# Kernel tuning notes

Measured on AMD Instinct MI355X. Metric: run time of the kernel, lower is better.

Reference implementation:

```python
import jax, jax.numpy as jnp
import numpy as np

N = 50000      # nodes
E = 800000     # edges
XS = 64        # x_size
ES = 32        # edge_attr dim (in_size = XS + ES = 96)
OUT = 64       # out_size
H = 128        # hidden_size
EPS = 1e-5


def _lin_init(k, fan_in, fan_out):
    s = 1.0 / np.sqrt(fan_in)
    kw, kb = jax.random.split(k)
    w = jax.random.uniform(kw, (fan_in, fan_out), minval=-s, maxval=s, dtype=jnp.float32)
    b = jax.random.uniform(kb, (fan_out,), minval=-s, maxval=s, dtype=jnp.float32)
    return w, b


def setup_inputs() -> dict:
    key = jax.random.key(0)
    ks = jax.random.split(key, 12)
    x = jax.random.normal(ks[0], (N, XS), dtype=jnp.float32)
    edge_index = jax.random.randint(ks[1], (2, E), 0, N, dtype=jnp.int64)
    edge_attr = jax.random.normal(ks[2], (E, ES), dtype=jnp.float32)
    u = jax.random.normal(ks[3], (1, 8), dtype=jnp.float32)
    batch = jnp.zeros((N,), dtype=jnp.int64)
    # MLP1: (96->128) LReLU (128->128) LReLU (128->64) LReLU LN(64)
    m1w0, m1b0 = _lin_init(ks[4], XS + ES, H)
    m1w1, m1b1 = _lin_init(ks[5], H, H)
    m1w2, m1b2 = _lin_init(ks[6], H, OUT)
    ln1_g = jnp.ones((OUT,), jnp.float32); ln1_b = jnp.zeros((OUT,), jnp.float32)
    # MLP2: (128->128) LReLU (128->128) LReLU (128->64) LReLU LN(64)
    m2w0, m2b0 = _lin_init(ks[7], XS + OUT, H)
    m2w1, m2b1 = _lin_init(ks[8], H, H)
    m2w2, m2b2 = _lin_init(ks[9], H, OUT)
    ln2_g = jnp.ones((OUT,), jnp.float32); ln2_b = jnp.zeros((OUT,), jnp.float32)
    return dict(x=x, edge_index=edge_index, edge_attr=edge_attr, u=u, batch=batch,
                m1w0=m1w0, m1b0=m1b0, m1w1=m1w1, m1b1=m1b1, m1w2=m1w2, m1b2=m1b2,
                ln1_g=ln1_g, ln1_b=ln1_b,
                m2w0=m2w0, m2b0=m2b0, m2w1=m2w1, m2b1=m2b1, m2w2=m2w2, m2b2=m2b2,
                ln2_g=ln2_g, ln2_b=ln2_b)


def _lrelu(v):
    return jax.nn.leaky_relu(v, 0.01)


def _layernorm(v, g, b):
    mu = jnp.mean(v, axis=-1, keepdims=True)
    var = jnp.mean(jnp.square(v - mu), axis=-1, keepdims=True)
    return (v - mu) * jax.lax.rsqrt(var + EPS) * g + b


def _mlp(h, w0, b0, w1, b1, w2, b2, g, bn):
    h = _lrelu(h @ w0 + b0)
    h = _lrelu(h @ w1 + b1)
    h = _lrelu(h @ w2 + b2)          # activate_last=True
    return _layernorm(h, g, bn)      # layer_norm=True


def reference(x, edge_index, edge_attr, u, batch,
              m1w0, m1b0, m1w1, m1b1, m1w2, m1b2, ln1_g, ln1_b,
              m2w0, m2b0, m2w1, m2b1, m2w2, m2b2, ln2_g, ln2_b):
    row, col = edge_index[0], edge_index[1]
    # gather source nodes, concat edge features -> per-edge MLP
    h = jnp.concatenate([x[row], edge_attr], axis=1)            # [E, 96]
    h = _mlp(h, m1w0, m1b0, m1w1, m1b1, m1w2, m1b2, ln1_g, ln1_b)  # [E, 64]
    # scatter_mean over destination nodes
    agg = jax.ops.segment_sum(h, col, num_segments=N)           # [N, 64]
    cnt = jax.ops.segment_sum(jnp.ones((E,), h.dtype), col, num_segments=N)
    agg = agg / jnp.maximum(cnt, 1.0)[:, None]
    # node update MLP
    h2 = jnp.concatenate([x, agg], axis=1)                      # [N, 128]
    return _mlp(h2, m2w0, m2b0, m2w1, m2b1, m2w2, m2b2, ln2_g, ln2_b)
```

## Files before the change

### kernel.cpp

```cpp
#include <hip/hip_runtime.h>


#define NNODES 50000
#define NEDGES 800000
#define NTILES_E 6250
#define NTILES_N 391

typedef __bf16 bf16;
typedef __bf16 __attribute__((ext_vector_type(4))) bf16x4;
typedef __bf16 __attribute__((ext_vector_type(8))) bf16x8;
typedef float __attribute__((ext_vector_type(4))) f32x4;

__device__ __forceinline__ f32x4 mfma_bf16(bf16x8 a, bf16x8 b, f32x4 c) {
    return __builtin_amdgcn_mfma_f32_16x16x32_bf16(a, b, c, 0, 0, 0);
}

__global__ void prep_weights(const float* __restrict__ w10, const float* __restrict__ w11,
                             const float* __restrict__ w12, const float* __restrict__ w20,
                             const float* __restrict__ w21, const float* __restrict__ w22,
                             bf16* __restrict__ img) {
    int idx = blockIdx.x * 256 + threadIdx.x;
    float f;
    if (idx < 13312) {
        int n = idx / 104, k = idx % 104;
        f = (k < 96) ? w10[k * 128 + n] : 0.0f;
    } else if (idx < 30720) {
        int t = idx - 13312; int n = t / 136, k = t % 136;
        f = (k < 128) ? w11[k * 128 + n] : 0.0f;
    } else if (idx < 39424) {
        int t = idx - 30720; int n = t / 136, k = t % 136;
        f = (k < 128) ? w12[k * 64 + n] : 0.0f;
    } else if (idx < 56832) {
        int t = idx - 39424; int n = t / 136, k = t % 136;
        f = (k < 128) ? w20[k * 128 + n] : 0.0f;
    } else if (idx < 74240) {
        int t = idx - 56832; int n = t / 136, k = t % 136;
        f = (k < 128) ? w21[k * 128 + n] : 0.0f;
    } else if (idx < 82944) {
        int t = idx - 74240; int n = t / 136, k = t % 136;
        f = (k < 128) ? w22[k * 64 + n] : 0.0f;
    } else {
        return;
    }
    img[idx] = (bf16)f;
}

__global__ void hist_kernel(const int* __restrict__ col, int* __restrict__ hist) {
    int i = blockIdx.x * 512 + threadIdx.x;
    if (i < NEDGES) atomicAdd(hist + col[i], 1);
}

__global__ void scanA(const int* __restrict__ hist, int* __restrict__ off,
                      int* __restrict__ csum) {
    __shared__ int sd[512];
    int t = threadIdx.x, i = blockIdx.x * 512 + t;
    int v = (i < NNODES) ? hist[i] : 0;
    sd[t] = v;
    __syncthreads();
    for (int o2 = 1; o2 < 512; o2 <<= 1) {
        int x = (t >= o2) ? sd[t - o2] : 0;
        __syncthreads();
        sd[t] += x;
        __syncthreads();
    }
    if (i < NNODES) off[i] = sd[t] - v;
    if (t == 511) csum[blockIdx.x] = sd[511];
}

__global__ void scanB(int* __restrict__ csum) {
    __shared__ int sd[128];
    int t = threadIdx.x;
    int v = (t < 98) ? csum[t] : 0;
    sd[t] = v;
    __syncthreads();
    for (int o2 = 1; o2 < 128; o2 <<= 1) {
        int x = (t >= o2) ? sd[t - o2] : 0;
        __syncthreads();
        sd[t] += x;
        __syncthreads();
    }
    if (t < 98) csum[t] = sd[t] - v;
}

__global__ void scanC(int* __restrict__ off, const int* __restrict__ csum) {
    int i = blockIdx.x * 512 + threadIdx.x;
    if (i < NNODES) off[i] += csum[blockIdx.x];
}

__global__ void scatter_kernel(const int* __restrict__ eidx, int* __restrict__ off,
                               int* __restrict__ perm, int* __restrict__ rdS) {
    int i = blockIdx.x * 512 + threadIdx.x;
    if (i < NEDGES) {
        int r = eidx[i], d = eidx[NEDGES + i];
        int pos = atomicAdd(off + d, 1);
        perm[pos] = i;
        rdS[pos] = r | (d << 16);
    }
}

__global__ __launch_bounds__(256) void edge_mlp(
    const float* __restrict__ x, const int* __restrict__ perm,
    const int* __restrict__ rdS, const float* __restrict__ eattr,
    const bf16* __restrict__ wimg,
    const float* __restrict__ b0g, const float* __restrict__ b1g,
    const float* __restrict__ b2g, const float* __restrict__ lng,
    const float* __restrict__ lnb, float* __restrict__ agg) {
    __shared__ __align__(16) bf16 wall[39424];
    __shared__ __align__(16) bf16 atile[128 * 104];
    __shared__ __align__(16) bf16 hid[128 * 136];
    __shared__ float bs[448];
    __shared__ int dstile[128];

    const int tid = threadIdx.x;
    {
        const uint4* src = (const uint4*)wimg;
        uint4* dst = (uint4*)wall;
        for (int i = tid; i < 4928; i += 256) dst[i] = src[i];
    }
    if (tid < 128) { bs[tid] = b0g[tid]; bs[128 + tid] = b1g[tid]; }
    else {
        int t = tid - 128;
        if (t < 64) { bs[256 + t] = b2g[t]; bs[320 + t] = lng[t]; bs[384 + t] = lnb[t]; }
    }
    __syncthreads();

    const int lane = tid & 63;
    const int wv = tid >> 6;
    const int col16 = lane & 15;
    const int quad = lane >> 4;

    float b0r[8], b1r[8], b2r[4], gr[4], br[4];
#pragma unroll
    for (int i = 0; i < 8; i++) { b0r[i] = bs[i * 16 + col16]; b1r[i] = bs[128 + i * 16 + col16]; }
#pragma unroll
    for (int i = 0; i < 4; i++) {
        b2r[i] = bs[256 + i * 16 + col16];
        gr[i] = bs[320 + i * 16 + col16];
        br[i] = bs[384 + i * 16 + col16];
    }

    const bf16* w0t = wall;
    const bf16* w1t = wall + 13312;
    const bf16* w2t = wall + 30720;

    const f32x4 vzero = {0.0f, 0.0f, 0.0f, 0.0f};
    const int r0 = wv * 32 + col16;
    const int rw = wv * 32 + quad * 4;
    const int el = tid >> 1, half = tid & 1;

    for (int tile = blockIdx.x; tile < NTILES_E; tile += gridDim.x) {
        const int sbase = tile * 128;
        {
            const int s = sbase + el;
            const int v = rdS[s];
            const int e = perm[s];
            const int r = v & 0xFFFF;
            if (half == 0) dstile[el] = ((unsigned)v) >> 16;
            const float4* xs = (const float4*)(x + (size_t)r * 64);
            bf16* arow = atile + el * 104;
#pragma unroll
            for (int j = 0; j < 8; j++) {
                float4 vv = xs[half * 8 + j];
                bf16x4 u = {(bf16)vv.x, (bf16)vv.y, (bf16)vv.z, (bf16)vv.w};
                *(bf16x4*)(arow + half * 32 + j * 4) = u;
            }
            const float4* es = (const float4*)(eattr + (size_t)e * 32);
#pragma unroll
            for (int j = 0; j < 4; j++) {
                float4 vv = es[half * 4 + j];
                bf16x4 u = {(bf16)vv.x, (bf16)vv.y, (bf16)vv.z, (bf16)vv.w};
                *(bf16x4*)(arow + 64 + half * 16 + j * 4) = u;
            }
        }

        f32x4 acc1[2][8];
#pragma unroll
        for (int mt = 0; mt < 2; mt++)
#pragma unroll
            for (int nt = 0; nt < 8; nt++) acc1[mt][nt] = vzero;
#pragma unroll
        for (int ks = 0; ks < 3; ks++) {
            bf16x8 a0 = *(const bf16x8*)(atile + r0 * 104 + ks * 32 + quad * 8);
            bf16x8 a1 = *(const bf16x8*)(atile + (r0 + 16) * 104 + ks * 32 + quad * 8);
#pragma unroll
            for (int nt = 0; nt < 8; nt++) {
                bf16x8 b = *(const bf16x8*)(w0t + (nt * 16 + col16) * 104 + ks * 32 + quad * 8);
                acc1[0][nt] = mfma_bf16(a0, b, acc1[0][nt]);
                acc1[1][nt] = mfma_bf16(a1, b, acc1[1][nt]);
            }
        }
#pragma unroll
        for (int mt = 0; mt < 2; mt++)
#pragma unroll
            for (int nt = 0; nt < 8; nt++)
#pragma unroll
                for (int rg = 0; rg < 4; rg++) {
                    float v = acc1[mt][nt][rg] + b0r[nt];
                    v = (v > 0.0f) ? v : 0.01f * v;
                    hid[(rw + mt * 16 + rg) * 136 + nt * 16 + col16] = (bf16)v;
                }

        bf16x8 a2[2][4];
#pragma unroll
        for (int mt = 0; mt < 2; mt++)
#pragma unroll
            for (int ks = 0; ks < 4; ks++)
                a2[mt][ks] = *(const bf16x8*)(hid + (r0 + mt * 16) * 136 + ks * 32 + quad * 8);
        f32x4 acc2[2][8];
#pragma unroll
        for (int mt = 0; mt < 2; mt++)
#pragma unroll
            for (int nt = 0; nt < 8; nt++) acc2[mt][nt] = vzero;
#pragma unroll
        for (int ks = 0; ks < 4; ks++) {
#pragma unroll
            for (int nt = 0; nt < 8; nt++) {
                bf16x8 b = *(const bf16x8*)(w1t + (nt * 16 + col16) * 136 + ks * 32 + quad * 8);
                acc2[0][nt] = mfma_bf16(a2[0][ks], b, acc2[0][nt]);
                acc2[1][nt] = mfma_bf16(a2[1][ks], b, acc2[1][nt]);
            }
        }
#pragma unroll
        for (int mt = 0; mt < 2; mt++)
#pragma unroll
            for (int nt = 0; nt < 8; nt++)
#pragma unroll
                for (int rg = 0; rg < 4; rg++) {
                    float v = acc2[mt][nt][rg] + b1r[nt];
                    v = (v > 0.0f) ? v : 0.01f * v;
                    hid[(rw + mt * 16 + rg) * 136 + nt * 16 + col16] = (bf16)v;
                }

        bf16x8 a3[2][4];
#pragma unroll
        for (int mt = 0; mt < 2; mt++)
#pragma unroll
            for (int ks = 0; ks < 4; ks++)
                a3[mt][ks] = *(const bf16x8*)(hid + (r0 + mt * 16) * 136 + ks * 32 + quad * 8);
        f32x4 acc3[2][4];
#pragma unroll
        for (int mt = 0; mt < 2; mt++)
#pragma unroll
            for (int nt = 0; nt < 4; nt++) acc3[mt][nt] = vzero;
#pragma unroll
        for (int ks = 0; ks < 4; ks++) {
#pragma unroll
            for (int nt = 0; nt < 4; nt++) {
                bf16x8 b = *(const bf16x8*)(w2t + (nt * 16 + col16) * 136 + ks * 32 + quad * 8);
                acc3[0][nt] = mfma_bf16(a3[0][ks], b, acc3[0][nt]);
                acc3[1][nt] = mfma_bf16(a3[1][ks], b, acc3[1][nt]);
            }
        }

#pragma unroll
        for (int mt = 0; mt < 2; mt++) {
            float vals[4][4];
            float s1[4] = {0.f, 0.f, 0.f, 0.f}, s2[4] = {0.f, 0.f, 0.f, 0.f};
#pragma unroll
            for (int nt = 0; nt < 4; nt++)
#pragma unroll
                for (int rg = 0; rg < 4; rg++) {
                    float v = acc3[mt][nt][rg] + b2r[nt];
                    v = (v > 0.0f) ? v : 0.01f * v;
                    vals[nt][rg] = v;
                    s1[rg] += v;
                    s2[rg] += v * v;
                }
#pragma unroll
            for (int off2 = 1; off2 < 16; off2 <<= 1) {
#pragma unroll
                for (int rg = 0; rg < 4; rg++) {
                    s1[rg] += __shfl_xor(s1[rg], off2);
                    s2[rg] += __shfl_xor(s2[rg], off2);
                }
            }
            float o[4][4];
            int dr[4];
#pragma unroll
            for (int rg = 0; rg < 4; rg++) {
                float mu = s1[rg] * 0.015625f;
                float var = s2[rg] * 0.015625f - mu * mu;
                float rstd = rsqrtf(var + 1e-5f);
                dr[rg] = dstile[rw + mt * 16 + rg];
#pragma unroll
                for (int nt = 0; nt < 4; nt++)
                    o[nt][rg] = (vals[nt][rg] - mu) * rstd * gr[nt] + br[nt];
            }
            float run0 = o[0][0], run1 = o[1][0], run2 = o[2][0], run3 = o[3][0];
            int cur = dr[0];
#pragma unroll
            for (int rg = 1; rg < 4; rg++) {
                if (dr[rg] != cur) {
                    float* dst = agg + (size_t)cur * 64 + col16;
                    atomicAdd(dst, run0); atomicAdd(dst + 16, run1);
                    atomicAdd(dst + 32, run2); atomicAdd(dst + 48, run3);
                    run0 = o[0][rg]; run1 = o[1][rg]; run2 = o[2][rg]; run3 = o[3][rg];
                    cur = dr[rg];
                } else {
                    run0 += o[0][rg]; run1 += o[1][rg]; run2 += o[2][rg]; run3 += o[3][rg];
                }
            }
            float* dst = agg + (size_t)cur * 64 + col16;
            atomicAdd(dst, run0); atomicAdd(dst + 16, run1);
            atomicAdd(dst + 32, run2); atomicAdd(dst + 48, run3);
        }
    }
}

__global__ __launch_bounds__(256) void node_mlp(
    const float* __restrict__ x, const float* __restrict__ agg,
    const int* __restrict__ hist, const bf16* __restrict__ wimg,
    const float* __restrict__ b0g, const float* __restrict__ b1g,
    const float* __restrict__ b2g, const float* __restrict__ lng,
    const float* __restrict__ lnb, float* __restrict__ out) {
    __shared__ __align__(16) bf16 wall[43520];
    __shared__ __align__(16) bf16 atile[128 * 136];
    __shared__ __align__(16) bf16 hid[128 * 136];
    __shared__ float bs[448];

    const int tid = threadIdx.x;
    {
        const uint4* src = (const uint4*)wimg;
        uint4* dst = (uint4*)wall;
        for (int i = tid; i < 5440; i += 256) dst[i] = src[i];
    }
    if (tid < 128) { bs[tid] = b0g[tid]; bs[128 + tid] = b1g[tid]; }
    else {
        int t = tid - 128;
        if (t < 64) { bs[256 + t] = b2g[t]; bs[320 + t] = lng[t]; bs[384 + t] = lnb[t]; }
    }
    __syncthreads();

    const int lane = tid & 63;
    const int wv = tid >> 6;
    const int col16 = lane & 15;
    const int quad = lane >> 4;

    float b0r[8], b1r[8], b2r[4], gr[4], br[4];
#pragma unroll
    for (int i = 0; i < 8; i++) { b0r[i] = bs[i * 16 + col16]; b1r[i] = bs[128 + i * 16 + col16]; }
#pragma unroll
    for (int i = 0; i < 4; i++) {
        b2r[i] = bs[256 + i * 16 + col16];
        gr[i] = bs[320 + i * 16 + col16];
        br[i] = bs[384 + i * 16 + col16];
    }

    const bf16* w0t = wall;
    const bf16* w1t = wall + 17408;
    const bf16* w2t = wall + 34816;

    const f32x4 vzero = {0.0f, 0.0f, 0.0f, 0.0f};
    const int r0 = wv * 32 + col16;
    const int rw = wv * 32 + quad * 4;
    const int el = tid >> 1, half = tid & 1;

    for (int tile = blockIdx.x; tile < NTILES_N; tile += gridDim.x) {
        const int nbase = tile * 128;
        {
            int i = nbase + el;
            if (i >= NNODES) i = NNODES - 1;
            const float4* xs = (const float4*)(x + (size_t)i * 64);
            bf16* arow = atile + el * 136;
#pragma unroll
            for (int j = 0; j < 8; j++) {
                float4 v = xs[half * 8 + j];
                bf16x4 u = {(bf16)v.x, (bf16)v.y, (bf16)v.z, (bf16)v.w};
                *(bf16x4*)(arow + half * 32 + j * 4) = u;
            }
            int c = hist[i];
            float inv = 1.0f / (float)(c > 1 ? c : 1);
            const float4* as = (const float4*)(agg + (size_t)i * 64);
#pragma unroll
            for (int j = 0; j < 8; j++) {
                float4 v = as[half * 8 + j];
                bf16x4 u = {(bf16)(v.x * inv), (bf16)(v.y * inv), (bf16)(v.z * inv), (bf16)(v.w * inv)};
                *(bf16x4*)(arow + 64 + half * 32 + j * 4) = u;
            }
        }

        f32x4 acc1[2][8];
#pragma unroll
        for (int mt = 0; mt < 2; mt++)
#pragma unroll
            for (int nt = 0; nt < 8; nt++) acc1[mt][nt] = vzero;
#pragma unroll
        for (int ks = 0; ks < 4; ks++) {
            bf16x8 a0 = *(const bf16x8*)(atile + r0 * 136 + ks * 32 + quad * 8);
            bf16x8 a1 = *(const bf16x8*)(atile + (r0 + 16) * 136 + ks * 32 + quad * 8);
#pragma unroll
            for (int nt = 0; nt < 8; nt++) {
                bf16x8 b = *(const bf16x8*)(w0t + (nt * 16 + col16) * 136 + ks * 32 + quad * 8);
                acc1[0][nt] = mfma_bf16(a0, b, acc1[0][nt]);
                acc1[1][nt] = mfma_bf16(a1, b, acc1[1][nt]);
            }
        }
#pragma unroll
        for (int mt = 0; mt < 2; mt++)
#pragma unroll
            for (int nt = 0; nt < 8; nt++)
#pragma unroll
                for (int rg = 0; rg < 4; rg++) {
                    float v = acc1[mt][nt][rg] + b0r[nt];
                    v = (v > 0.0f) ? v : 0.01f * v;
                    hid[(rw + mt * 16 + rg) * 136 + nt * 16 + col16] = (bf16)v;
                }

        bf16x8 a2[2][4];
#pragma unroll
        for (int mt = 0; mt < 2; mt++)
#pragma unroll
            for (int ks = 0; ks < 4; ks++)
                a2[mt][ks] = *(const bf16x8*)(hid + (r0 + mt * 16) * 136 + ks * 32 + quad * 8);
        f32x4 acc2[2][8];
#pragma unroll
        for (int mt = 0; mt < 2; mt++)
#pragma unroll
            for (int nt = 0; nt < 8; nt++) acc2[mt][nt] = vzero;
#pragma unroll
        for (int ks = 0; ks < 4; ks++) {
#pragma unroll
            for (int nt = 0; nt < 8; nt++) {
                bf16x8 b = *(const bf16x8*)(w1t + (nt * 16 + col16) * 136 + ks * 32 + quad * 8);
                acc2[0][nt] = mfma_bf16(a2[0][ks], b, acc2[0][nt]);
                acc2[1][nt] = mfma_bf16(a2[1][ks], b, acc2[1][nt]);
            }
        }
#pragma unroll
        for (int mt = 0; mt < 2; mt++)
#pragma unroll
            for (int nt = 0; nt < 8; nt++)
#pragma unroll
                for (int rg = 0; rg < 4; rg++) {
                    float v = acc2[mt][nt][rg] + b1r[nt];
                    v = (v > 0.0f) ? v : 0.01f * v;
                    hid[(rw + mt * 16 + rg) * 136 + nt * 16 + col16] = (bf16)v;
                }

        bf16x8 a3[2][4];
#pragma unroll
        for (int mt = 0; mt < 2; mt++)
#pragma unroll
            for (int ks = 0; ks < 4; ks++)
                a3[mt][ks] = *(const bf16x8*)(hid + (r0 + mt * 16) * 136 + ks * 32 + quad * 8);
        f32x4 acc3[2][4];
#pragma unroll
        for (int mt = 0; mt < 2; mt++)
#pragma unroll
            for (int nt = 0; nt < 4; nt++) acc3[mt][nt] = vzero;
#pragma unroll
        for (int ks = 0; ks < 4; ks++) {
#pragma unroll
            for (int nt = 0; nt < 4; nt++) {
                bf16x8 b = *(const bf16x8*)(w2t + (nt * 16 + col16) * 136 + ks * 32 + quad * 8);
                acc3[0][nt] = mfma_bf16(a3[0][ks], b, acc3[0][nt]);
                acc3[1][nt] = mfma_bf16(a3[1][ks], b, acc3[1][nt]);
            }
        }

#pragma unroll
        for (int mt = 0; mt < 2; mt++) {
            float vals[4][4];
            float s1[4] = {0.f, 0.f, 0.f, 0.f}, s2[4] = {0.f, 0.f, 0.f, 0.f};
#pragma unroll
            for (int nt = 0; nt < 4; nt++)
#pragma unroll
                for (int rg = 0; rg < 4; rg++) {
                    float v = acc3[mt][nt][rg] + b2r[nt];
                    v = (v > 0.0f) ? v : 0.01f * v;
                    vals[nt][rg] = v;
                    s1[rg] += v;
                    s2[rg] += v * v;
                }
#pragma unroll
            for (int off2 = 1; off2 < 16; off2 <<= 1) {
#pragma unroll
                for (int rg = 0; rg < 4; rg++) {
                    s1[rg] += __shfl_xor(s1[rg], off2);
                    s2[rg] += __shfl_xor(s2[rg], off2);
                }
            }
#pragma unroll
            for (int rg = 0; rg < 4; rg++) {
                float mu = s1[rg] * 0.015625f;
                float var = s2[rg] * 0.015625f - mu * mu;
                float rstd = rsqrtf(var + 1e-5f);
                int i = nbase + rw + mt * 16 + rg;
                if (i < NNODES) {
#pragma unroll
                    for (int nt = 0; nt < 4; nt++) {
                        float o = (vals[nt][rg] - mu) * rstd * gr[nt] + br[nt];
                        out[(size_t)i * 64 + nt * 16 + col16] = o;
                    }
                }
            }
        }
    }
}

extern "C" void kernel_launch(void* const* d_in, const int* in_sizes, int n_in,
                              void* d_out, int out_size, void* d_ws, size_t ws_size,
                              hipStream_t stream) {
    (void)in_sizes; (void)n_in; (void)out_size; (void)ws_size;
    const float* x     = (const float*)d_in[0];
    const int*   eidx  = (const int*)d_in[1];
    const float* eattr = (const float*)d_in[2];
    const float* m1w0 = (const float*)d_in[5];
    const float* m1b0 = (const float*)d_in[6];
    const float* m1w1 = (const float*)d_in[7];
    const float* m1b1 = (const float*)d_in[8];
    const float* m1w2 = (const float*)d_in[9];
    const float* m1b2 = (const float*)d_in[10];
    const float* ln1g = (const float*)d_in[11];
    const float* ln1b = (const float*)d_in[12];
    const float* m2w0 = (const float*)d_in[13];
    const float* m2b0 = (const float*)d_in[14];
    const float* m2w1 = (const float*)d_in[15];
    const float* m2b1 = (const float*)d_in[16];
    const float* m2w2 = (const float*)d_in[17];
    const float* m2b2 = (const float*)d_in[18];
    const float* ln2g = (const float*)d_in[19];
    const float* ln2b = (const float*)d_in[20];

    char* ws = (char*)d_ws;
    float* agg  = (float*)ws;
    int*   hist = (int*)(ws + 12800000);
    int*   off  = (int*)(ws + 13000000);
    int*   csum = (int*)(ws + 13200000);
    int*   perm = (int*)(ws + 13200512);
    int*   rdS  = (int*)(ws + 16400512);
    bf16*  wimg = (bf16*)(ws + 19600512);

    hipMemsetAsync(d_ws, 0, 13000000, stream);
    prep_weights<<<324, 256, 0, stream>>>(m1w0, m1w1, m1w2, m2w0, m2w1, m2w2, wimg);
    hist_kernel<<<1563, 512, 0, stream>>>(eidx + NEDGES, hist);
    scanA<<<98, 512, 0, stream>>>(hist, off, csum);
    scanB<<<1, 128, 0, stream>>>(csum);
    scanC<<<98, 512, 0, stream>>>(off, csum);
    scatter_kernel<<<1563, 512, 0, stream>>>(eidx, off, perm, rdS);
    edge_mlp<<<512, 256, 0, stream>>>(x, perm, rdS, eattr, wimg, m1b0, m1b1, m1b2,
                                      ln1g, ln1b, agg);
    node_mlp<<<196, 256, 0, stream>>>(x, agg, hist, wimg + 39424,
                                      m2b0, m2b1, m2b2, ln2g, ln2b, (float*)d_out);
}
```

Baseline: 532.8 us.

## Read MFMA-fragment weights from global memory and launch one tile per block

Weights are pre-swizzled into MFMA fragment order so each lane loads its B operand directly from global/L2 instead of staging ~79KB of weights in LDS per block. With LDS shrunk, blocks become one-shot (6250 edge blocks, 391 node blocks) with launch_bounds for two blocks per SM, raising occupancy. The perm and rdS arrays are merged into one int2 array, and destination ids are fetched via a wave shuffle instead of LDS. The tradeoff is repeated global weight loads per tile, which rely on cache hits, in exchange for dropping the per-block weight-copy prologue and gaining occupancy.

```diff
diff --git a/kernel.cpp b/kernel.cpp
--- a/kernel.cpp
+++ b/kernel.cpp
@@ -3,8 +3,6 @@
 
 #define NNODES 50000
 #define NEDGES 800000
-#define NTILES_E 6250
-#define NTILES_N 391
 
 typedef __bf16 bf16;
 typedef __bf16 __attribute__((ext_vector_type(4))) bf16x4;
@@ -20,29 +18,20 @@
                              const float* __restrict__ w21, const float* __restrict__ w22,
                              bf16* __restrict__ img) {
     int idx = blockIdx.x * 256 + threadIdx.x;
-    float f;
-    if (idx < 13312) {
-        int n = idx / 104, k = idx % 104;
-        f = (k < 96) ? w10[k * 128 + n] : 0.0f;
-    } else if (idx < 30720) {
-        int t = idx - 13312; int n = t / 136, k = t % 136;
-        f = (k < 128) ? w11[k * 128 + n] : 0.0f;
-    } else if (idx < 39424) {
-        int t = idx - 30720; int n = t / 136, k = t % 136;
-        f = (k < 128) ? w12[k * 64 + n] : 0.0f;
-    } else if (idx < 56832) {
-        int t = idx - 39424; int n = t / 136, k = t % 136;
-        f = (k < 128) ? w20[k * 128 + n] : 0.0f;
-    } else if (idx < 74240) {
-        int t = idx - 56832; int n = t / 136, k = t % 136;
-        f = (k < 128) ? w21[k * 128 + n] : 0.0f;
-    } else if (idx < 82944) {
-        int t = idx - 74240; int n = t / 136, k = t % 136;
-        f = (k < 128) ? w22[k * 64 + n] : 0.0f;
-    } else {
-        return;
-    }
-    img[idx] = (bf16)f;
+    if (idx >= 77824) return;
+    const float* w; int N; int t;
+    if (idx < 12288)      { w = w10; N = 128; t = idx; }
+    else if (idx < 28672) { w = w11; N = 128; t = idx - 12288; }
+    else if (idx < 36864) { w = w12; N = 64;  t = idx - 28672; }
+    else if (idx < 53248) { w = w20; N = 128; t = idx - 36864; }
+    else if (idx < 69632) { w = w21; N = 128; t = idx - 53248; }
+    else                  { w = w22; N = 64;  t = idx - 69632; }
+    int j = t & 7, lane = (t >> 3) & 63, blk = t >> 9;
+    int NT = N >> 4;
+    int nt = blk % NT, ks = blk / NT;
+    int k = ks * 32 + ((lane >> 4) << 3) + j;
+    int n = nt * 16 + (lane & 15);
+    img[idx] = (bf16)w[k * N + n];
 }
 
 __global__ void hist_kernel(const int* __restrict__ col, int* __restrict__ hist) {
@@ -88,42 +77,25 @@
 }
 
 __global__ void scatter_kernel(const int* __restrict__ eidx, int* __restrict__ off,
-                               int* __restrict__ perm, int* __restrict__ rdS) {
+                               int2* __restrict__ prd) {
     int i = blockIdx.x * 512 + threadIdx.x;
     if (i < NEDGES) {
         int r = eidx[i], d = eidx[NEDGES + i];
         int pos = atomicAdd(off + d, 1);
-        perm[pos] = i;
-        rdS[pos] = r | (d << 16);
-    }
-}
-
-__global__ __launch_bounds__(256) void edge_mlp(
-    const float* __restrict__ x, const int* __restrict__ perm,
-    const int* __restrict__ rdS, const float* __restrict__ eattr,
-    const bf16* __restrict__ wimg,
+        prd[pos] = make_int2(i, r | (d << 16));
+    }
+}
+
+__global__ __launch_bounds__(256, 2) void edge_mlp(
+    const float* __restrict__ x, const int2* __restrict__ prd,
+    const float* __restrict__ eattr, const bf16* __restrict__ wimg,
     const float* __restrict__ b0g, const float* __restrict__ b1g,
     const float* __restrict__ b2g, const float* __restrict__ lng,
     const float* __restrict__ lnb, float* __restrict__ agg) {
-    __shared__ __align__(16) bf16 wall[39424];
     __shared__ __align__(16) bf16 atile[128 * 104];
     __shared__ __align__(16) bf16 hid[128 * 136];
-    __shared__ float bs[448];
-    __shared__ int dstile[128];
 
     const int tid = threadIdx.x;
-    {
-        const uint4* src = (const uint4*)wimg;
-        uint4* dst = (uint4*)wall;
-        for (int i = tid; i < 4928; i += 256) dst[i] = src[i];
-    }
-    if (tid < 128) { bs[tid] = b0g[tid]; bs[128 + tid] = b1g[tid]; }
-    else {
-        int t = tid - 128;
-        if (t < 64) { bs[256 + t] = b2g[t]; bs[320 + t] = lng[t]; bs[384 + t] = lnb[t]; }
-    }
-    __syncthreads();
-
     const int lane = tid & 63;
     const int wv = tid >> 6;
     const int col16 = lane & 15;
@@ -131,206 +103,186 @@
 
     float b0r[8], b1r[8], b2r[4], gr[4], br[4];
 #pragma unroll
-    for (int i = 0; i < 8; i++) { b0r[i] = bs[i * 16 + col16]; b1r[i] = bs[128 + i * 16 + col16]; }
+    for (int i = 0; i < 8; i++) { b0r[i] = b0g[i * 16 + col16]; b1r[i] = b1g[i * 16 + col16]; }
 #pragma unroll
     for (int i = 0; i < 4; i++) {
-        b2r[i] = bs[256 + i * 16 + col16];
-        gr[i] = bs[320 + i * 16 + col16];
-        br[i] = bs[384 + i * 16 + col16];
-    }
-
-    const bf16* w0t = wall;
-    const bf16* w1t = wall + 13312;
-    const bf16* w2t = wall + 30720;
-
+        b2r[i] = b2g[i * 16 + col16];
+        gr[i] = lng[i * 16 + col16];
+        br[i] = lnb[i * 16 + col16];
+    }
+
+    const bf16* wl = wimg + (size_t)lane * 8;
     const f32x4 vzero = {0.0f, 0.0f, 0.0f, 0.0f};
     const int r0 = wv * 32 + col16;
     const int rw = wv * 32 + quad * 4;
-    const int el = tid >> 1, half = tid & 1;
-
-    for (int tile = blockIdx.x; tile < NTILES_E; tile += gridDim.x) {
-        const int sbase = tile * 128;
-        {
-            const int s = sbase + el;
-            const int v = rdS[s];
-            const int e = perm[s];
-            const int r = v & 0xFFFF;
-            if (half == 0) dstile[el] = ((unsigned)v) >> 16;
-            const float4* xs = (const float4*)(x + (size_t)r * 64);
-            bf16* arow = atile + el * 104;
-#pragma unroll
-            for (int j = 0; j < 8; j++) {
-                float4 vv = xs[half * 8 + j];
-                bf16x4 u = {(bf16)vv.x, (bf16)vv.y, (bf16)vv.z, (bf16)vv.w};
-                *(bf16x4*)(arow + half * 32 + j * 4) = u;
-            }
-            const float4* es = (const float4*)(eattr + (size_t)e * 32);
-#pragma unroll
-            for (int j = 0; j < 4; j++) {
-                float4 vv = es[half * 4 + j];
-                bf16x4 u = {(bf16)vv.x, (bf16)vv.y, (bf16)vv.z, (bf16)vv.w};
-                *(bf16x4*)(arow + 64 + half * 16 + j * 4) = u;
-            }
-        }
-
-        f32x4 acc1[2][8];
-#pragma unroll
-        for (int mt = 0; mt < 2; mt++)
-#pragma unroll
-            for (int nt = 0; nt < 8; nt++) acc1[mt][nt] = vzero;
-#pragma unroll
-        for (int ks = 0; ks < 3; ks++) {
-            bf16x8 a0 = *(const bf16x8*)(atile + r0 * 104 + ks * 32 + quad * 8);
-            bf16x8 a1 = *(const bf16x8*)(atile + (r0 + 16) * 104 + ks * 32 + quad * 8);
-#pragma unroll
-            for (int nt = 0; nt < 8; nt++) {
-                bf16x8 b = *(const bf16x8*)(w0t + (nt * 16 + col16) * 104 + ks * 32 + quad * 8);
-                acc1[0][nt] = mfma_bf16(a0, b, acc1[0][nt]);
-                acc1[1][nt] = mfma_bf16(a1, b, acc1[1][nt]);
-            }
-        }
-#pragma unroll
-        for (int mt = 0; mt < 2; mt++)
-#pragma unroll
-            for (int nt = 0; nt < 8; nt++)
-#pragma unroll
-                for (int rg = 0; rg < 4; rg++) {
-                    float v = acc1[mt][nt][rg] + b0r[nt];
-                    v = (v > 0.0f) ? v : 0.01f * v;
-                    hid[(rw + mt * 16 + rg) * 136 + nt * 16 + col16] = (bf16)v;
-                }
-
-        bf16x8 a2[2][4];
-#pragma unroll
-        for (int mt = 0; mt < 2; mt++)
-#pragma unroll
-            for (int ks = 0; ks < 4; ks++)
-                a2[mt][ks] = *(const bf16x8*)(hid + (r0 + mt * 16) * 136 + ks * 32 + quad * 8);
-        f32x4 acc2[2][8];
-#pragma unroll
-        for (int mt = 0; mt < 2; mt++)
-#pragma unroll
-            for (int nt = 0; nt < 8; nt++) acc2[mt][nt] = vzero;
-#pragma unroll
-        for (int ks = 0; ks < 4; ks++) {
-#pragma unroll
-            for (int nt = 0; nt < 8; nt++) {
-                bf16x8 b = *(const bf16x8*)(w1t + (nt * 16 + col16) * 136 + ks * 32 + quad * 8);
-                acc2[0][nt] = mfma_bf16(a2[0][ks], b, acc2[0][nt]);
-                acc2[1][nt] = mfma_bf16(a2[1][ks], b, acc2[1][nt]);
-            }
-        }
-#pragma unroll
-        for (int mt = 0; mt < 2; mt++)
-#pragma unroll
-            for (int nt = 0; nt < 8; nt++)
-#pragma unroll
-                for (int rg = 0; rg < 4; rg++) {
-                    float v = acc2[mt][nt][rg] + b1r[nt];
-                    v = (v > 0.0f) ? v : 0.01f * v;
-                    hid[(rw + mt * 16 + rg) * 136 + nt * 16 + col16] = (bf16)v;
-                }
-
-        bf16x8 a3[2][4];
-#pragma unroll
-        for (int mt = 0; mt < 2; mt++)
-#pragma unroll
-            for (int ks = 0; ks < 4; ks++)
-                a3[mt][ks] = *(const bf16x8*)(hid + (r0 + mt * 16) * 136 + ks * 32 + quad * 8);
-        f32x4 acc3[2][4];
-#pragma unroll
-        for (int mt = 0; mt < 2; mt++)
-#pragma unroll
-            for (int nt = 0; nt < 4; nt++) acc3[mt][nt] = vzero;
-#pragma unroll
-        for (int ks = 0; ks < 4; ks++) {
-#pragma unroll
-            for (int nt = 0; nt < 4; nt++) {
-                bf16x8 b = *(const bf16x8*)(w2t + (nt * 16 + col16) * 136 + ks * 32 + quad * 8);
-                acc3[0][nt] = mfma_bf16(a3[0][ks], b, acc3[0][nt]);
-                acc3[1][nt] = mfma_bf16(a3[1][ks], b, acc3[1][nt]);
-            }
-        }
-
-#pragma unroll
-        for (int mt = 0; mt < 2; mt++) {
-            float vals[4][4];
-            float s1[4] = {0.f, 0.f, 0.f, 0.f}, s2[4] = {0.f, 0.f, 0.f, 0.f};
+    const int sbase = blockIdx.x * 128;
+
+    int vreg;
+    {
+        const int el = tid >> 1, half = tid & 1;
+        int2 v = prd[sbase + el];
+        vreg = v.y;
+        const int r = v.y & 0xFFFF;
+        const float4* xs = (const float4*)(x + (size_t)r * 64);
+        bf16* arow = atile + el * 104;
+#pragma unroll
+        for (int j = 0; j < 8; j++) {
+            float4 vv = xs[half * 8 + j];
+            bf16x4 u = {(bf16)vv.x, (bf16)vv.y, (bf16)vv.z, (bf16)vv.w};
+            *(bf16x4*)(arow + half * 32 + j * 4) = u;
+        }
+        const float4* es = (const float4*)(eattr + (size_t)v.x * 32);
+#pragma unroll
+        for (int j = 0; j < 4; j++) {
+            float4 vv = es[half * 4 + j];
+            bf16x4 u = {(bf16)vv.x, (bf16)vv.y, (bf16)vv.z, (bf16)vv.w};
+            *(bf16x4*)(arow + 64 + half * 16 + j * 4) = u;
+        }
+    }
+
+    f32x4 acc1[2][8];
+#pragma unroll
+    for (int mt = 0; mt < 2; mt++)
+#pragma unroll
+        for (int nt = 0; nt < 8; nt++) acc1[mt][nt] = vzero;
+#pragma unroll
+    for (int ks = 0; ks < 3; ks++) {
+        bf16x8 a0 = *(const bf16x8*)(atile + r0 * 104 + ks * 32 + quad * 8);
+        bf16x8 a1 = *(const bf16x8*)(atile + (r0 + 16) * 104 + ks * 32 + quad * 8);
+#pragma unroll
+        for (int nt = 0; nt < 8; nt++) {
+            bf16x8 b = *(const bf16x8*)(wl + (ks * 8 + nt) * 512);
+            acc1[0][nt] = mfma_bf16(a0, b, acc1[0][nt]);
+            acc1[1][nt] = mfma_bf16(a1, b, acc1[1][nt]);
+        }
+    }
+#pragma unroll
+    for (int mt = 0; mt < 2; mt++)
+#pragma unroll
+        for (int nt = 0; nt < 8; nt++)
+#pragma unroll
+            for (int rg = 0; rg < 4; rg++) {
+                float v = acc1[mt][nt][rg] + b0r[nt];
+                v = (v > 0.0f) ? v : 0.01f * v;
+                hid[(rw + mt * 16 + rg) * 136 + nt * 16 + col16] = (bf16)v;
+            }
+
+    bf16x8 a2[2][4];
+#pragma unroll
+    for (int mt = 0; mt < 2; mt++)
+#pragma unroll
+        for (int ks = 0; ks < 4; ks++)
+            a2[mt][ks] = *(const bf16x8*)(hid + (r0 + mt * 16) * 136 + ks * 32 + quad * 8);
+    f32x4 acc2[2][8];
+#pragma unroll
+    for (int mt = 0; mt < 2; mt++)
+#pragma unroll
+        for (int nt = 0; nt < 8; nt++) acc2[mt][nt] = vzero;
+#pragma unroll
+    for (int ks = 0; ks < 4; ks++) {
+#pragma unroll
+        for (int nt = 0; nt < 8; nt++) {
+            bf16x8 b = *(const bf16x8*)(wl + 12288 + (ks * 8 + nt) * 512);
+            acc2[0][nt] = mfma_bf16(a2[0][ks], b, acc2[0][nt]);
+            acc2[1][nt] = mfma_bf16(a2[1][ks], b, acc2[1][nt]);
+        }
+    }
+#pragma unroll
+    for (int mt = 0; mt < 2; mt++)
+#pragma unroll
+        for (int nt = 0; nt < 8; nt++)
+#pragma unroll
+            for (int rg = 0; rg < 4; rg++) {
+                float v = acc2[mt][nt][rg] + b1r[nt];
+                v = (v > 0.0f) ? v : 0.01f * v;
+                hid[(rw + mt * 16 + rg) * 136 + nt * 16 + col16] = (bf16)v;
+            }
+
+    bf16x8 a3[2][4];
+#pragma unroll
+    for (int mt = 0; mt < 2; mt++)
+#pragma unroll
+        for (int ks = 0; ks < 4; ks++)
+            a3[mt][ks] = *(const bf16x8*)(hid + (r0 + mt * 16) * 136 + ks * 32 + quad * 8);
+    f32x4 acc3[2][4];
+#pragma unroll
+    for (int mt = 0; mt < 2; mt++)
+#pragma unroll
+        for (int nt = 0; nt < 4; nt++) acc3[mt][nt] = vzero;
+#pragma unroll
+    for (int ks = 0; ks < 4; ks++) {
+#pragma unroll
+        for (int nt = 0; nt < 4; nt++) {
+            bf16x8 b = *(const bf16x8*)(wl + 28672 + (ks * 4 + nt) * 512);
+            acc3[0][nt] = mfma_bf16(a3[0][ks], b, acc3[0][nt]);
+            acc3[1][nt] = mfma_bf16(a3[1][ks], b, acc3[1][nt]);
+        }
+    }
+
+#pragma unroll
+    for (int mt = 0; mt < 2; mt++) {
+        float vals[4][4];
+        float s1[4] = {0.f, 0.f, 0.f, 0.f}, s2[4] = {0.f, 0.f, 0.f, 0.f};
+#pragma unroll
+        for (int nt = 0; nt < 4; nt++)
+#pragma unroll
+            for (int rg = 0; rg < 4; rg++) {
+                float v = acc3[mt][nt][rg] + b2r[nt];
+                v = (v > 0.0f) ? v : 0.01f * v;
+                vals[nt][rg] = v;
+                s1[rg] += v;
+                s2[rg] += v * v;
+            }
+#pragma unroll
+        for (int off2 = 1; off2 < 16; off2 <<= 1) {
+#pragma unroll
+            for (int rg = 0; rg < 4; rg++) {
+                s1[rg] += __shfl_xor(s1[rg], off2);
+                s2[rg] += __shfl_xor(s2[rg], off2);
+            }
+        }
+        float o[4][4];
+        int dr[4];
+#pragma unroll
+        for (int rg = 0; rg < 4; rg++) {
+            float mu = s1[rg] * 0.015625f;
+            float var = s2[rg] * 0.015625f - mu * mu;
+            float rstd = rsqrtf(var + 1e-5f);
+            dr[rg] = ((unsigned)__shfl(vreg, (mt * 16 + quad * 4 + rg) << 1)) >> 16;
 #pragma unroll
             for (int nt = 0; nt < 4; nt++)
-#pragma unroll
-                for (int rg = 0; rg < 4; rg++) {
-                    float v = acc3[mt][nt][rg] + b2r[nt];
-                    v = (v > 0.0f) ? v : 0.01f * v;
-                    vals[nt][rg] = v;
-                    s1[rg] += v;
-                    s2[rg] += v * v;
-                }
-#pragma unroll
-            for (int off2 = 1; off2 < 16; off2 <<= 1) {
-#pragma unroll
-                for (int rg = 0; rg < 4; rg++) {
-                    s1[rg] += __shfl_xor(s1[rg], off2);
-                    s2[rg] += __shfl_xor(s2[rg], off2);
-                }
-            }
-            float o[4][4];
-            int dr[4];
-#pragma unroll
-            for (int rg = 0; rg < 4; rg++) {
-                float mu = s1[rg] * 0.015625f;
-                float var = s2[rg] * 0.015625f - mu * mu;
-                float rstd = rsqrtf(var + 1e-5f);
-                dr[rg] = dstile[rw + mt * 16 + rg];
-#pragma unroll
-                for (int nt = 0; nt < 4; nt++)
-                    o[nt][rg] = (vals[nt][rg] - mu) * rstd * gr[nt] + br[nt];
-            }
-            float run0 = o[0][0], run1 = o[1][0], run2 = o[2][0], run3 = o[3][0];
-            int cur = dr[0];
-#pragma unroll
-            for (int rg = 1; rg < 4; rg++) {
-                if (dr[rg] != cur) {
-                    float* dst = agg + (size_t)cur * 64 + col16;
-                    atomicAdd(dst, run0); atomicAdd(dst + 16, run1);
-                    atomicAdd(dst + 32, run2); atomicAdd(dst + 48, run3);
-                    run0 = o[0][rg]; run1 = o[1][rg]; run2 = o[2][rg]; run3 = o[3][rg];
-                    cur = dr[rg];
-                } else {
-                    run0 += o[0][rg]; run1 += o[1][rg]; run2 += o[2][rg]; run3 += o[3][rg];
-                }
-            }
-            float* dst = agg + (size_t)cur * 64 + col16;
-            atomicAdd(dst, run0); atomicAdd(dst + 16, run1);
-            atomicAdd(dst + 32, run2); atomicAdd(dst + 48, run3);
-        }
-    }
-}
-
-__global__ __launch_bounds__(256) void node_mlp(
+                o[nt][rg] = (vals[nt][rg] - mu) * rstd * gr[nt] + br[nt];
+        }
+        float run0 = o[0][0], run1 = o[1][0], run2 = o[2][0], run3 = o[3][0];
+        int cur = dr[0];
+#pragma unroll
+        for (int rg = 1; rg < 4; rg++) {
+            if (dr[rg] != cur) {
+                float* dst = agg + (size_t)cur * 64 + col16;
+                atomicAdd(dst, run0); atomicAdd(dst + 16, run1);
+                atomicAdd(dst + 32, run2); atomicAdd(dst + 48, run3);
+                run0 = o[0][rg]; run1 = o[1][rg]; run2 = o[2][rg]; run3 = o[3][rg];
+                cur = dr[rg];
+            } else {
+                run0 += o[0][rg]; run1 += o[1][rg]; run2 += o[2][rg]; run3 += o[3][rg];
+            }
+        }
+        float* dst = agg + (size_t)cur * 64 + col16;
+        atomicAdd(dst, run0); atomicAdd(dst + 16, run1);
+        atomicAdd(dst + 32, run2); atomicAdd(dst + 48, run3);
+    }
+}
+
+__global__ __launch_bounds__(256, 2) void node_mlp(
     const float* __restrict__ x, const float* __restrict__ agg,
     const int* __restrict__ hist, const bf16* __restrict__ wimg,
     const float* __restrict__ b0g, const float* __restrict__ b1g,
     const float* __restrict__ b2g, const float* __restrict__ lng,
     const float* __restrict__ lnb, float* __restrict__ out) {
-    __shared__ __align__(16) bf16 wall[43520];
     __shared__ __align__(16) bf16 atile[128 * 136];
     __shared__ __align__(16) bf16 hid[128 * 136];
-    __shared__ float bs[448];
 
     const int tid = threadIdx.x;
-    {
-        const uint4* src = (const uint4*)wimg;
-        uint4* dst = (uint4*)wall;
-        for (int i = tid; i < 5440; i += 256) dst[i] = src[i];
-    }
-    if (tid < 128) { bs[tid] = b0g[tid]; bs[128 + tid] = b1g[tid]; }
-    else {
-        int t = tid - 128;
-        if (t < 64) { bs[256 + t] = b2g[t]; bs[320 + t] = lng[t]; bs[384 + t] = lnb[t]; }
-    }
-    __syncthreads();
-
     const int lane = tid & 63;
     const int wv = tid >> 6;
     const int col16 = lane & 15;
@@ -338,160 +290,155 @@
 
     float b0r[8], b1r[8], b2r[4], gr[4], br[4];
 #pragma unroll
-    for (int i = 0; i < 8; i++) { b0r[i] = bs[i * 16 + col16]; b1r[i] = bs[128 + i * 16 + col16]; }
+    for (int i = 0; i < 8; i++) { b0r[i] = b0g[i * 16 + col16]; b1r[i] = b1g[i * 16 + col16]; }
 #pragma unroll
     for (int i = 0; i < 4; i++) {
-        b2r[i] = bs[256 + i * 16 + col16];
-        gr[i] = bs[320 + i * 16 + col16];
-        br[i] = bs[384 + i * 16 + col16];
-    }
-
-    const bf16* w0t = wall;
-    const bf16* w1t = wall + 17408;
-    const bf16* w2t = wall + 34816;
-
+        b2r[i] = b2g[i * 16 + col16];
+        gr[i] = lng[i * 16 + col16];
+        br[i] = lnb[i * 16 + col16];
+    }
+
+    const bf16* wl = wimg + 36864 + (size_t)lane * 8;
     const f32x4 vzero = {0.0f, 0.0f, 0.0f, 0.0f};
     const int r0 = wv * 32 + col16;
     const int rw = wv * 32 + quad * 4;
-    const int el = tid >> 1, half = tid & 1;
-
-    for (int tile = blockIdx.x; tile < NTILES_N; tile += gridDim.x) {
-        const int nbase = tile * 128;
-        {
-            int i = nbase + el;
-            if (i >= NNODES) i = NNODES - 1;
-            const float4* xs = (const float4*)(x + (size_t)i * 64);
-            bf16* arow = atile + el * 136;
-#pragma unroll
-            for (int j = 0; j < 8; j++) {
-                float4 v = xs[half * 8 + j];
-                bf16x4 u = {(bf16)v.x, (bf16)v.y, (bf16)v.z, (bf16)v.w};
-                *(bf16x4*)(arow + half * 32 + j * 4) = u;
-            }
-            int c = hist[i];
-            float inv = 1.0f / (float)(c > 1 ? c : 1);
-            const float4* as = (const float4*)(agg + (size_t)i * 64);
-#pragma unroll
-            for (int j = 0; j < 8; j++) {
-                float4 v = as[half * 8 + j];
-                bf16x4 u = {(bf16)(v.x * inv), (bf16)(v.y * inv), (bf16)(v.z * inv), (bf16)(v.w * inv)};
-                *(bf16x4*)(arow + 64 + half * 32 + j * 4) = u;
-            }
-        }
-
-        f32x4 acc1[2][8];
-#pragma unroll
-        for (int mt = 0; mt < 2; mt++)
-#pragma unroll
-            for (int nt = 0; nt < 8; nt++) acc1[mt][nt] = vzero;
-#pragma unroll
-        for (int ks = 0; ks < 4; ks++) {
-            bf16x8 a0 = *(const bf16x8*)(atile + r0 * 136 + ks * 32 + quad * 8);
-            bf16x8 a1 = *(const bf16x8*)(atile + (r0 + 16) * 136 + ks * 32 + quad * 8);
-#pragma unroll
-            for (int nt = 0; nt < 8; nt++) {
-                bf16x8 b = *(const bf16x8*)(w0t + (nt * 16 + col16) * 136 + ks * 32 + quad * 8);
-                acc1[0][nt] = mfma_bf16(a0, b, acc1[0][nt]);
-                acc1[1][nt] = mfma_bf16(a1, b, acc1[1][nt]);
-            }
-        }
-#pragma unroll
-        for (int mt = 0; mt < 2; mt++)
-#pragma unroll
-            for (int nt = 0; nt < 8; nt++)
-#pragma unroll
-                for (int rg = 0; rg < 4; rg++) {
-                    float v = acc1[mt][nt][rg] + b0r[nt];
-                    v = (v > 0.0f) ? v : 0.01f * v;
-                    hid[(rw + mt * 16 + rg) * 136 + nt * 16 + col16] = (bf16)v;
-                }
-
-        bf16x8 a2[2][4];
-#pragma unroll
-        for (int mt = 0; mt < 2; mt++)
-#pragma unroll
-            for (int ks = 0; ks < 4; ks++)
-                a2[mt][ks] = *(const bf16x8*)(hid + (r0 + mt * 16) * 136 + ks * 32 + quad * 8);
-        f32x4 acc2[2][8];
-#pragma unroll
-        for (int mt = 0; mt < 2; mt++)
-#pragma unroll
-            for (int nt = 0; nt < 8; nt++) acc2[mt][nt] = vzero;
-#pragma unroll
-        for (int ks = 0; ks < 4; ks++) {
-#pragma unroll
-            for (int nt = 0; nt < 8; nt++) {
-                bf16x8 b = *(const bf16x8*)(w1t + (nt * 16 + col16) * 136 + ks * 32 + quad * 8);
-                acc2[0][nt] = mfma_bf16(a2[0][ks], b, acc2[0][nt]);
-                acc2[1][nt] = mfma_bf16(a2[1][ks], b, acc2[1][nt]);
-            }
-        }
-#pragma unroll
-        for (int mt = 0; mt < 2; mt++)
-#pragma unroll
-            for (int nt = 0; nt < 8; nt++)
-#pragma unroll
-                for (int rg = 0; rg < 4; rg++) {
-                    float v = acc2[mt][nt][rg] + b1r[nt];
-                    v = (v > 0.0f) ? v : 0.01f * v;
-                    hid[(rw + mt * 16 + rg) * 136 + nt * 16 + col16] = (bf16)v;
-                }
-
-        bf16x8 a3[2][4];
-#pragma unroll
-        for (int mt = 0; mt < 2; mt++)
-#pragma unroll
-            for (int ks = 0; ks < 4; ks++)
-                a3[mt][ks] = *(const bf16x8*)(hid + (r0 + mt * 16) * 136 + ks * 32 + quad * 8);
-        f32x4 acc3[2][4];
-#pragma unroll
-        for (int mt = 0; mt < 2; mt++)
-#pragma unroll
-            for (int nt = 0; nt < 4; nt++) acc3[mt][nt] = vzero;
-#pragma unroll
-        for (int ks = 0; ks < 4; ks++) {
-#pragma unroll
-            for (int nt = 0; nt < 4; nt++) {
-                bf16x8 b = *(const bf16x8*)(w2t + (nt * 16 + col16) * 136 + ks * 32 + quad * 8);
-                acc3[0][nt] = mfma_bf16(a3[0][ks], b, acc3[0][nt]);
-                acc3[1][nt] = mfma_bf16(a3[1][ks], b, acc3[1][nt]);
-            }
-        }
-
-#pragma unroll
-        for (int mt = 0; mt < 2; mt++) {
-            float vals[4][4];
-            float s1[4] = {0.f, 0.f, 0.f, 0.f}, s2[4] = {0.f, 0.f, 0.f, 0.f};
-#pragma unroll
-            for (int nt = 0; nt < 4; nt++)
-#pragma unroll
-                for (int rg = 0; rg < 4; rg++) {
-                    float v = acc3[mt][nt][rg] + b2r[nt];
-                    v = (v > 0.0f) ? v : 0.01f * v;
-                    vals[nt][rg] = v;
-                    s1[rg] += v;
-                    s2[rg] += v * v;
-                }
-#pragma unroll
-            for (int off2 = 1; off2 < 16; off2 <<= 1) {
-#pragma unroll
-                for (int rg = 0; rg < 4; rg++) {
-                    s1[rg] += __shfl_xor(s1[rg], off2);
-                    s2[rg] += __shfl_xor(s2[rg], off2);
-                }
-            }
-#pragma unroll
-            for (int rg = 0; rg < 4; rg++) {
-                float mu = s1[rg] * 0.015625f;
-                float var = s2[rg] * 0.015625f - mu * mu;
-                float rstd = rsqrtf(var + 1e-5f);
-                int i = nbase + rw + mt * 16 + rg;
-                if (i < NNODES) {
-#pragma unroll
-                    for (int nt = 0; nt < 4; nt++) {
-                        float o = (vals[nt][rg] - mu) * rstd * gr[nt] + br[nt];
-                        out[(size_t)i * 64 + nt * 16 + col16] = o;
-                    }
+    const int nbase = blockIdx.x * 128;
+
+    {
+        const int el = tid >> 1, half = tid & 1;
+        int i = nbase + el;
+        if (i >= NNODES) i = NNODES - 1;
+        const float4* xs = (const float4*)(x + (size_t)i * 64);
+        bf16* arow = atile + el * 136;
+#pragma unroll
+        for (int j = 0; j < 8; j++) {
+            float4 v = xs[half * 8 + j];
+            bf16x4 u = {(bf16)v.x, (bf16)v.y, (bf16)v.z, (bf16)v.w};
+            *(bf16x4*)(arow + half * 32 + j * 4) = u;
+        }
+        int c = hist[i];
+        float inv = 1.0f / (float)(c > 1 ? c : 1);
+        const float4* as = (const float4*)(agg + (size_t)i * 64);
+#pragma unroll
+        for (int j = 0; j < 8; j++) {
+            float4 v = as[half * 8 + j];
+            bf16x4 u = {(bf16)(v.x * inv), (bf16)(v.y * inv), (bf16)(v.z * inv), (bf16)(v.w * inv)};
+            *(bf16x4*)(arow + 64 + half * 32 + j * 4) = u;
+        }
+    }
+
+    f32x4 acc1[2][8];
+#pragma unroll
+    for (int mt = 0; mt < 2; mt++)
+#pragma unroll
+        for (int nt = 0; nt < 8; nt++) acc1[mt][nt] = vzero;
+#pragma unroll
+    for (int ks = 0; ks < 4; ks++) {
+        bf16x8 a0 = *(const bf16x8*)(atile + r0 * 136 + ks * 32 + quad * 8);
+        bf16x8 a1 = *(const bf16x8*)(atile + (r0 + 16) * 136 + ks * 32 + quad * 8);
+#pragma unroll
+        for (int nt = 0; nt < 8; nt++) {
+            bf16x8 b = *(const bf16x8*)(wl + (ks * 8 + nt) * 512);
+            acc1[0][nt] = mfma_bf16(a0, b, acc1[0][nt]);
+            acc1[1][nt] = mfma_bf16(a1, b, acc1[1][nt]);
+        }
+    }
+#pragma unroll
+    for (int mt = 0; mt < 2; mt++)
+#pragma unroll
+        for (int nt = 0; nt < 8; nt++)
+#pragma unroll
+            for (int rg = 0; rg < 4; rg++) {
+                float v = acc1[mt][nt][rg] + b0r[nt];
+                v = (v > 0.0f) ? v : 0.01f * v;
+                hid[(rw + mt * 16 + rg) * 136 + nt * 16 + col16] = (bf16)v;
+            }
+
+    bf16x8 a2[2][4];
+#pragma unroll
+    for (int mt = 0; mt < 2; mt++)
+#pragma unroll
+        for (int ks = 0; ks < 4; ks++)
+            a2[mt][ks] = *(const bf16x8*)(hid + (r0 + mt * 16) * 136 + ks * 32 + quad * 8);
+    f32x4 acc2[2][8];
+#pragma unroll
+    for (int mt = 0; mt < 2; mt++)
+#pragma unroll
+        for (int nt = 0; nt < 8; nt++) acc2[mt][nt] = vzero;
+#pragma unroll
+    for (int ks = 0; ks < 4; ks++) {
+#pragma unroll
+        for (int nt = 0; nt < 8; nt++) {
+            bf16x8 b = *(const bf16x8*)(wl + 16384 + (ks * 8 + nt) * 512);
+            acc2[0][nt] = mfma_bf16(a2[0][ks], b, acc2[0][nt]);
+            acc2[1][nt] = mfma_bf16(a2[1][ks], b, acc2[1][nt]);
+        }
+    }
+#pragma unroll
+    for (int mt = 0; mt < 2; mt++)
+#pragma unroll
+        for (int nt = 0; nt < 8; nt++)
+#pragma unroll
+            for (int rg = 0; rg < 4; rg++) {
+                float v = acc2[mt][nt][rg] + b1r[nt];
+                v = (v > 0.0f) ? v : 0.01f * v;
+                hid[(rw + mt * 16 + rg) * 136 + nt * 16 + col16] = (bf16)v;
+            }
+
+    bf16x8 a3[2][4];
+#pragma unroll
+    for (int mt = 0; mt < 2; mt++)
+#pragma unroll
+        for (int ks = 0; ks < 4; ks++)
+            a3[mt][ks] = *(const bf16x8*)(hid + (r0 + mt * 16) * 136 + ks * 32 + quad * 8);
+    f32x4 acc3[2][4];
+#pragma unroll
+    for (int mt = 0; mt < 2; mt++)
+#pragma unroll
+        for (int nt = 0; nt < 4; nt++) acc3[mt][nt] = vzero;
+#pragma unroll
+    for (int ks = 0; ks < 4; ks++) {
+#pragma unroll
+        for (int nt = 0; nt < 4; nt++) {
+            bf16x8 b = *(const bf16x8*)(wl + 32768 + (ks * 4 + nt) * 512);
+            acc3[0][nt] = mfma_bf16(a3[0][ks], b, acc3[0][nt]);
+            acc3[1][nt] = mfma_bf16(a3[1][ks], b, acc3[1][nt]);
+        }
+    }
+
+#pragma unroll
+    for (int mt = 0; mt < 2; mt++) {
+        float vals[4][4];
+        float s1[4] = {0.f, 0.f, 0.f, 0.f}, s2[4] = {0.f, 0.f, 0.f, 0.f};
+#pragma unroll
+        for (int nt = 0; nt < 4; nt++)
+#pragma unroll
+            for (int rg = 0; rg < 4; rg++) {
+                float v = acc3[mt][nt][rg] + b2r[nt];
+                v = (v > 0.0f) ? v : 0.01f * v;
+                vals[nt][rg] = v;
+                s1[rg] += v;
+                s2[rg] += v * v;
+            }
+#pragma unroll
+        for (int off2 = 1; off2 < 16; off2 <<= 1) {
+#pragma unroll
+            for (int rg = 0; rg < 4; rg++) {
+                s1[rg] += __shfl_xor(s1[rg], off2);
+                s2[rg] += __shfl_xor(s2[rg], off2);
+            }
+        }
+#pragma unroll
+        for (int rg = 0; rg < 4; rg++) {
+            float mu = s1[rg] * 0.015625f;
+            float var = s2[rg] * 0.015625f - mu * mu;
+            float rstd = rsqrtf(var + 1e-5f);
+            int i = nbase + rw + mt * 16 + rg;
+            if (i < NNODES) {
+#pragma unroll
+                for (int nt = 0; nt < 4; nt++) {
+                    float o = (vals[nt][rg] - mu) * rstd * gr[nt] + br[nt];
+                    out[(size_t)i * 64 + nt * 16 + col16] = o;
                 }
             }
         }
@@ -527,19 +474,18 @@
     int*   hist = (int*)(ws + 12800000);
     int*   off  = (int*)(ws + 13000000);
     int*   csum = (int*)(ws + 13200000);
-    int*   perm = (int*)(ws + 13200512);
-    int*   rdS  = (int*)(ws + 16400512);
+    int2*  prd  = (int2*)(ws + 13200512);
     bf16*  wimg = (bf16*)(ws + 19600512);
 
     hipMemsetAsync(d_ws, 0, 13000000, stream);
-    prep_weights<<<324, 256, 0, stream>>>(m1w0, m1w1, m1w2, m2w0, m2w1, m2w2, wimg);
+    prep_weights<<<304, 256, 0, stream>>>(m1w0, m1w1, m1w2, m2w0, m2w1, m2w2, wimg);
     hist_kernel<<<1563, 512, 0, stream>>>(eidx + NEDGES, hist);
     scanA<<<98, 512, 0, stream>>>(hist, off, csum);
     scanB<<<1, 128, 0, stream>>>(csum);
     scanC<<<98, 512, 0, stream>>>(off, csum);
-    scatter_kernel<<<1563, 512, 0, stream>>>(eidx, off, perm, rdS);
-    edge_mlp<<<512, 256, 0, stream>>>(x, perm, rdS, eattr, wimg, m1b0, m1b1, m1b2,
-                                      ln1g, ln1b, agg);
-    node_mlp<<<196, 256, 0, stream>>>(x, agg, hist, wimg + 39424,
+    scatter_kernel<<<1563, 512, 0, stream>>>(eidx, off, prd);
+    edge_mlp<<<6250, 256, 0, stream>>>(x, prd, eattr, wimg, m1b0, m1b1, m1b2,
+                                       ln1g, ln1b, agg);
+    node_mlp<<<391, 256, 0, stream>>>(x, agg, hist, wimg,
                                       m2b0, m2b1, m2b2, ln2g, ln2b, (float*)d_out);
 }
```

After: 558.9 us. +4.9%, slower.
